# Optimization experiments

Hardware: AMD Instinct MI355X
Metric: run time of the kernel (lower is better)

Reference implementation:

```python
import jax, jax.numpy as jnp
from jax import lax
import numpy as np

B, H, W, C = 16, 128, 256, 64
D = 12            # local_max_disp // stride
H_OUT, W_OUT = 1024, 2048


def setup_inputs() -> dict:
    key = jax.random.key(0)
    ks = jax.random.split(key, 8)
    feat_l = jax.random.normal(ks[0], (B, H, W, C), dtype=jnp.float32)
    feat_r = jax.random.normal(ks[1], (B, H, W, C), dtype=jnp.float32)
    def conv_w(k, shape):
        fan_in = shape[0] * shape[1] * shape[2] * shape[3]
        return jax.random.normal(k, shape, dtype=jnp.float32) / np.sqrt(fan_in)
    return {
        'feat_l': feat_l, 'feat_r': feat_r,
        'w0': conv_w(ks[2], (3, 3, 3, 1, 4)), 'b0': jnp.zeros((4,), jnp.float32),
        'w1': conv_w(ks[3], (3, 3, 3, 4, 4)), 'b1': jnp.zeros((4,), jnp.float32),
        'w2': conv_w(ks[4], (3, 3, 3, 4, 4)), 'b2': jnp.zeros((4,), jnp.float32),
        'w3': conv_w(ks[5], (3, 3, 3, 4, 4)), 'b3': jnp.zeros((4,), jnp.float32),
        'wf': conv_w(ks[6], (3, 3, 3, 4, 1)), 'bf': jnp.zeros((1,), jnp.float32),
    }


def _cost_volume(feat_l, feat_r, max_disp, stride):
    # For disparity i: cost[:, :, w, i] = sum_c |L[b,h,w,c] - R[b,h,w-i,c]| for w >= i,
    # and sum_c |L[b,h,w,c]| for w < i (which equals diff against a zero-padded shift of R).
    planes = []
    for i in range(0, max_disp, stride):
        if i == 0:
            r_shift = feat_r
        else:
            r_shift = jnp.pad(feat_r[:, :, :-i, :], ((0, 0), (0, 0), (i, 0), (0, 0)))
        planes.append(jnp.sum(jnp.abs(feat_l - r_shift), axis=-1))
    return jnp.stack(planes, axis=-1)  # [B,H,W,D]


def _conv3d(x, w, b):
    # x: [B,H,W,D,C_in], w: [3,3,3,C_in,C_out]
    y = lax.conv_general_dilated(x, w, (1, 1, 1), 'SAME',
                                 dimension_numbers=('NHWDC', 'HWDIO', 'NHWDC'))
    return y + b


def reference(feat_l, feat_r, w0, b0, w1, b1, w2, b2, w3, b3, wf, bf):
    cost = _cost_volume(feat_l, feat_r, D, 1)          # [B,H,W,D]
    x = cost[..., None]                                 # [B,H,W,D,1]
    x = jax.nn.relu(_conv3d(x, w0, b0))
    x = jax.nn.relu(_conv3d(x, w1, b1))
    x = jax.nn.relu(_conv3d(x, w2, b2))
    x = jax.nn.relu(_conv3d(x, w3, b3))
    x = _conv3d(x, wf, bf)                              # [B,H,W,D,1]
    cost = x[..., 0]                                    # [B,H,W,D]
    sm = jax.nn.softmax(-cost, axis=-1)
    disp = jnp.arange(D, dtype=jnp.float32)
    pred = jnp.sum(sm * disp, axis=-1, keepdims=True)   # [B,H,W,1]
    out = jax.image.resize(pred, (pred.shape[0], H_OUT, W_OUT, 1), method='bilinear')
    return out
```

## Files before the change

### kernel.cpp

```cpp
#include <hip/hip_runtime.h>
#include <cstddef>

#define BB   16
#define HHY  128
#define WWX  256
#define CC   64
#define DDp  12
#define HOUT 1024
#define WOUT 2048

typedef _Float16 hf;
typedef __fp16 h2 __attribute__((ext_vector_type(2)));

__device__ __forceinline__ h2 u2h(unsigned u) { return __builtin_bit_cast(h2, u); }
__device__ __forceinline__ unsigned pkrtz(float a, float b) {
  return __builtin_bit_cast(unsigned, __builtin_amdgcn_cvt_pkrtz(a, b));
}

#if defined(__has_builtin)
#if __has_builtin(__builtin_amdgcn_fdot2)
#define FDOT2(a, b, c) __builtin_amdgcn_fdot2((a), (b), (c), false)
#endif
#endif
#ifndef FDOT2
#define FDOT2(a, b, c) ((float)(a)[0] * (float)(b)[0] + (float)(a)[1] * (float)(b)[1] + (c))
#endif

__device__ __forceinline__ float adot(unsigned lu, unsigned ru, float c) {
  const h2 d = u2h(lu) - u2h(ru);
  const unsigned au = __builtin_bit_cast(unsigned, d) & 0x7FFF7FFFu;
  return FDOT2(u2h(au), u2h(0x3C003C00u), c);
}

__global__ __launch_bounds__(256) void prep_k(const float* __restrict__ w1,
                                              const float* __restrict__ w2,
                                              const float* __restrict__ w3,
                                              const float* __restrict__ wf,
                                              hf* __restrict__ o) {
  const int t = threadIdx.x;
  for (int i = t; i < 432; i += 256) {
    const int t27 = i >> 4;
    const int ci = (i >> 2) & 3;
    const int co = i & 3;
    const int dst = (t27 * 4 + co) * 4 + ci;
    o[dst]       = (hf)w1[i];
    o[432 + dst] = (hf)w2[i];
    o[864 + dst] = (hf)w3[i];
  }
  for (int i = t; i < 108; i += 256) o[1296 + i] = (hf)wf[i];
}

#define RSTRIDE 36

__global__ __launch_bounds__(256) void cost_volume_k(const float* __restrict__ L,
                                                     const float* __restrict__ R,
                                                     float* __restrict__ cost) {
  __shared__ unsigned lsR[WWX * RSTRIDE];
  const int t = threadIdx.x;
  const int h = blockIdx.x;
  const int b = blockIdx.y;
  const size_t rowbase = ((size_t)(b * HHY + h)) * WWX;
  const float* Lrow = L + rowbase * CC;
  const float* Rrow = R + rowbase * CC;

#pragma unroll
  for (int j = 0; j < 16; ++j) {
    const int fi = t + 256 * j;
    const int w = fi >> 4;
    const int f4 = fi & 15;
    const float4 v = *(const float4*)(Rrow + (size_t)w * CC + 4 * f4);
    *(uint2*)(&lsR[w * RSTRIDE + f4 * 2]) =
        make_uint2(pkrtz(v.x, v.y), pkrtz(v.z, v.w));
  }

  unsigned lh[32];
#pragma unroll
  for (int k = 0; k < 16; ++k) {
    const float4 v = *(const float4*)(Lrow + (size_t)t * CC + 4 * k);
    lh[2 * k]     = pkrtz(v.x, v.y);
    lh[2 * k + 1] = pkrtz(v.z, v.w);
  }

  float sl = 0.f;
#pragma unroll
  for (int i = 0; i < 32; ++i) sl = adot(lh[i], 0u, sl);

  __syncthreads();

  float acc[DDp];
#pragma unroll
  for (int d = 0; d < DDp; ++d) {
    if (t >= d) {
      const unsigned* rp = &lsR[(t - d) * RSTRIDE];
      float a = 0.f;
#pragma unroll
      for (int k = 0; k < 8; ++k) {
        const uint4 r = *(const uint4*)(rp + 4 * k);
        a = adot(lh[4 * k + 0], r.x, a);
        a = adot(lh[4 * k + 1], r.y, a);
        a = adot(lh[4 * k + 2], r.z, a);
        a = adot(lh[4 * k + 3], r.w, a);
      }
      acc[d] = a;
    } else {
      acc[d] = sl;
    }
  }

  float* cp = cost + (rowbase + t) * DDp;
#pragma unroll
  for (int d = 0; d < DDp; d += 4)
    *(float4*)(cp + d) = make_float4(acc[d], acc[d + 1], acc[d + 2], acc[d + 3]);
}

__global__ __launch_bounds__(256) void conv0_k(const float* __restrict__ x,
                                               const float* __restrict__ wt,
                                               const float* __restrict__ bs,
                                               hf* __restrict__ y) {
  constexpr int S = 20;
  __shared__ float ls[WWX * S];
  const int t = threadIdx.x;
  const int id = blockIdx.x;
  const int h = ((id & 7) << 4) | ((id >> 3) & 15);
  const int b = id >> 7;

  float acc[DDp][4];
#pragma unroll
  for (int co = 0; co < 4; ++co) {
    const float bv = bs[co];
#pragma unroll
    for (int d = 0; d < DDp; ++d) acc[d][co] = bv;
  }

#pragma unroll
  for (int kh = 0; kh < 3; ++kh) {
    const int hh = h + kh - 1;
    if (hh < 0 || hh >= HHY) continue;

    __syncthreads();
    const float* xr = x + ((size_t)(b * HHY + hh) * WWX) * DDp;
#pragma unroll
    for (int j = 0; j < 3; ++j) {
      const int fi4 = t + 256 * j;
      const int w_ = fi4 / 3;
      const int k_ = fi4 - w_ * 3;
      *(float4*)(&ls[w_ * S + k_ * 4]) = ((const float4*)xr)[fi4];
    }
    __syncthreads();

#pragma unroll
    for (int kw = 0; kw < 3; ++kw) {
      const int ww = t + kw - 1;
      if (ww < 0 || ww >= WWX) continue;
      const float* lp = &ls[ww * S];

      const float* wp = wt + (size_t)(kh * 3 + kw) * 12;
      float wr[12];
#pragma unroll
      for (int i = 0; i < 12; ++i) wr[i] = wp[i];

      float v[DDp];
#pragma unroll
      for (int k = 0; k < 3; ++k)
        ((float4*)v)[k] = *(const float4*)(lp + 4 * k);
#pragma unroll
      for (int vo = 0; vo < DDp; ++vo)
#pragma unroll
        for (int kd = 0; kd < 3; ++kd) {
          const int d = vo + 1 - kd;
          if (d < 0 || d >= DDp) continue;
#pragma unroll
          for (int co = 0; co < 4; ++co)
            acc[d][co] += v[vo] * wr[kd * 4 + co];
        }
    }
  }

  unsigned ov[DDp * 2];
#pragma unroll
  for (int d = 0; d < DDp; ++d) {
    ov[d * 2]     = pkrtz(fmaxf(acc[d][0], 0.f), fmaxf(acc[d][1], 0.f));
    ov[d * 2 + 1] = pkrtz(fmaxf(acc[d][2], 0.f), fmaxf(acc[d][3], 0.f));
  }
  uint4* yp = (uint4*)(y + ((size_t)(b * HHY + h) * WWX + t) * (DDp * 4));
#pragma unroll
  for (int i = 0; i < 6; ++i) yp[i] = ((uint4*)ov)[i];
}

template <int COUT, bool FUSE_SM>
__global__ __launch_bounds__(256) void convh_k(const hf* __restrict__ x,
                                               const hf* __restrict__ wh,
                                               const float* __restrict__ bs,
                                               void* __restrict__ yv) {
  constexpr int DCH = DDp * 4;
  constexpr int SU  = 26;
  __shared__ unsigned lsu[WWX * SU];

  const int t = threadIdx.x;
  const int id = blockIdx.x;
  const int h = ((id & 7) << 4) | ((id >> 3) & 15);
  const int b = id >> 7;

  float acc[DDp][COUT];
#pragma unroll
  for (int co = 0; co < COUT; ++co) {
    const float bv = bs[co];
#pragma unroll
    for (int d = 0; d < DDp; ++d) acc[d][co] = bv;
  }

  const unsigned* whu = (const unsigned*)wh;

#pragma unroll
  for (int kh = 0; kh < 3; ++kh) {
    const int hh = h + kh - 1;
    if (hh < 0 || hh >= HHY) continue;

    __syncthreads();
    const uint4* xr = (const uint4*)(x + (size_t)(b * HHY + hh) * WWX * DCH);
#pragma unroll
    for (int j = 0; j < 6; ++j) {
      const int fi4 = t + 256 * j;
      const int w_ = fi4 / 6;
      const int k_ = fi4 - w_ * 6;
      const uint4 v = xr[fi4];
      unsigned* dst = &lsu[w_ * SU + k_ * 4];
      *(uint2*)(dst)     = make_uint2(v.x, v.y);
      *(uint2*)(dst + 2) = make_uint2(v.z, v.w);
    }
    __syncthreads();

#pragma unroll
    for (int kw = 0; kw < 3; ++kw) {
      const int ww = t + kw - 1;
      if (ww < 0 || ww >= WWX) continue;

      unsigned w01[3][COUT], w23[3][COUT];
      const int tap3 = (kh * 3 + kw) * 3;
#pragma unroll
      for (int kd = 0; kd < 3; ++kd)
#pragma unroll
        for (int co = 0; co < COUT; ++co) {
          const int u0 = ((tap3 + kd) * COUT + co) * 2;
          w01[kd][co] = whu[u0];
          w23[kd][co] = whu[u0 + 1];
        }

      const unsigned* lp = &lsu[ww * SU];
#pragma unroll
      for (int vo = 0; vo < DDp; ++vo) {
        const uint2 xu = *(const uint2*)(lp + vo * 2);
        const h2 x01 = u2h(xu.x), x23 = u2h(xu.y);
#pragma unroll
        for (int kd = 0; kd < 3; ++kd) {
          const int d = vo + 1 - kd;
          if (d < 0 || d >= DDp) continue;
#pragma unroll
          for (int co = 0; co < COUT; ++co)
            acc[d][co] = FDOT2(x01, u2h(w01[kd][co]),
                         FDOT2(x23, u2h(w23[kd][co]), acc[d][co]));
        }
      }
    }
  }

  if constexpr (FUSE_SM) {
    float* y = (float*)yv;
    float mn = acc[0][0];
#pragma unroll
    for (int d = 1; d < DDp; ++d) mn = fminf(mn, acc[d][0]);
    float s = 0.f, sw = 0.f;
#pragma unroll
    for (int d = 0; d < DDp; ++d) {
      const float e = __expf(mn - acc[d][0]);
      s += e;
      sw += e * (float)d;
    }
    y[(size_t)(b * HHY + h) * WWX + t] = sw / s;
  } else {
    hf* y = (hf*)yv;
    unsigned ov[DDp * 2];
#pragma unroll
    for (int d = 0; d < DDp; ++d) {
      ov[d * 2]     = pkrtz(fmaxf(acc[d][0], 0.f), fmaxf(acc[d][1 % COUT], 0.f));
      ov[d * 2 + 1] = pkrtz(fmaxf(acc[d][2 % COUT], 0.f), fmaxf(acc[d][3 % COUT], 0.f));
    }
    uint4* yp = (uint4*)(y + ((size_t)(b * HHY + h) * WWX + t) * DCH);
#pragma unroll
    for (int i = 0; i < 6; ++i) yp[i] = ((uint4*)ov)[i];
  }
}

__global__ __launch_bounds__(256) void resize4_k(const float* __restrict__ pred,
                                                 float* __restrict__ out) {
  const int idx = blockIdx.x * 256 + threadIdx.x;
  const int xg = idx & 511;
  const int y = (idx >> 9) & 1023;
  const int b = idx >> 19;

  const int parity = xg & 1;
  const int m = xg >> 1;
  const int x0 = m - 1 + parity;
  const int x0c = max(x0, 0);
  const int x1c = min(x0 + 1, WWX - 1);
  const float wx0 = (parity ? 0.0625f : 0.5625f);

  const int py = y & 7;
  const int my = y >> 3;
  const int y0 = my - 1 + (py >= 4 ? 1 : 0);
  const float wy = (py >= 4) ? 0.0625f + (py - 4) * 0.125f : 0.5625f + py * 0.125f;
  const int y0c = max(y0, 0);
  const int y1c = min(y0 + 1, HHY - 1);

  const float* pb = pred + (size_t)b * HHY * WWX;
  const float a = pb[y0c * WWX + x0c];
  const float bv = pb[y0c * WWX + x1c];
  const float c = pb[y1c * WWX + x0c];
  const float d = pb[y1c * WWX + x1c];

  const float top0 = a + (bv - a) * wx0;
  const float bot0 = c + (d - c) * wx0;
  const float dtop = (bv - a) * 0.125f;
  const float dbot = (d - c) * 0.125f;

  float4 o;
  o.x = top0 + wy * (bot0 - top0);
  o.y = (top0 + dtop) + wy * ((bot0 + dbot) - (top0 + dtop));
  o.z = (top0 + 2.f * dtop) + wy * ((bot0 + 2.f * dbot) - (top0 + 2.f * dtop));
  o.w = (top0 + 3.f * dtop) + wy * ((bot0 + 3.f * dbot) - (top0 + 3.f * dtop));

  *(float4*)(out + (size_t)idx * 4) = o;
}

extern "C" void kernel_launch(void* const* d_in, const int* in_sizes, int n_in,
                              void* d_out, int out_size, void* d_ws, size_t ws_size,
                              hipStream_t stream) {
  const float* feat_l = (const float*)d_in[0];
  const float* feat_r = (const float*)d_in[1];
  const float* w0 = (const float*)d_in[2];
  const float* b0 = (const float*)d_in[3];
  const float* w1 = (const float*)d_in[4];
  const float* b1 = (const float*)d_in[5];
  const float* w2 = (const float*)d_in[6];
  const float* b2 = (const float*)d_in[7];
  const float* w3 = (const float*)d_in[8];
  const float* b3 = (const float*)d_in[9];
  const float* wf = (const float*)d_in[10];
  const float* bf = (const float*)d_in[11];
  float* out = (float*)d_out;

  char* ws = (char*)d_ws;
  hf*    A  = (hf*)ws;
  hf*    Bf = (hf*)(ws + 50331648);
  float* C  = (float*)(ws + 100663296);
  float* P  = (float*)(ws + 125829120);
  hf*    Wh = (hf*)(ws + 127926272);

  dim3 blk(256);
  prep_k<<<dim3(1), blk, 0, stream>>>(w1, w2, w3, wf, Wh);
  cost_volume_k<<<dim3(HHY, BB), blk, 0, stream>>>(feat_l, feat_r, C);
  conv0_k<<<dim3(HHY * BB), blk, 0, stream>>>(C, w0, b0, A);
  convh_k<4, false><<<dim3(HHY * BB), blk, 0, stream>>>(A,  Wh,        b1, Bf);
  convh_k<4, false><<<dim3(HHY * BB), blk, 0, stream>>>(Bf, Wh + 432,  b2, A);
  convh_k<4, false><<<dim3(HHY * BB), blk, 0, stream>>>(A,  Wh + 864,  b3, Bf);
  convh_k<1, true ><<<dim3(HHY * BB), blk, 0, stream>>>(Bf, Wh + 1296, bf, P);

  const int ngroups = BB * HOUT * (WOUT / 4);
  resize4_k<<<dim3(ngroups / 256), blk, 0, stream>>>(P, out);
}
```

Baseline: 299.5 us.

## Tile cost volume along width and split disparities across thread groups

The cost volume kernel now launches one block per 64-column tile of a row instead of one per full row, staging the R halo and the L tile as fp16 in shared memory. Each thread computes three disparities for one column rather than twelve, and results are transposed through LDS for coalesced float4 stores. The goal is more blocks, less LDS per block and fewer registers, which raises occupancy and shortens per-thread serial work. In exchange, L rows are re-read from LDS by four thread groups, the R halo is loaded redundantly per tile, and two extra barriers are added.

```diff
diff --git a/kernel.cpp b/kernel.cpp
--- a/kernel.cpp
+++ b/kernel.cpp
@@ -50,67 +50,75 @@
   for (int i = t; i < 108; i += 256) o[1296 + i] = (hf)wf[i];
 }
 
-#define RSTRIDE 36
-
-__global__ __launch_bounds__(256) void cost_volume_k(const float* __restrict__ L,
-                                                     const float* __restrict__ R,
-                                                     float* __restrict__ cost) {
-  __shared__ unsigned lsR[WWX * RSTRIDE];
+#define CVS 36
+#define CVHALO 11
+#define CVWT 64
+#define CVROWS (CVWT + CVHALO + CVWT)
+
+__global__ __launch_bounds__(256, 8) void cost_volume_k(const float* __restrict__ L,
+                                                        const float* __restrict__ R,
+                                                        float* __restrict__ cost) {
+  __shared__ unsigned ls[CVROWS * CVS];
   const int t = threadIdx.x;
-  const int h = blockIdx.x;
-  const int b = blockIdx.y;
+  const int wb = blockIdx.x * CVWT;
+  const int h = blockIdx.y;
+  const int b = blockIdx.z;
   const size_t rowbase = ((size_t)(b * HHY + h)) * WWX;
   const float* Lrow = L + rowbase * CC;
   const float* Rrow = R + rowbase * CC;
 
 #pragma unroll
-  for (int j = 0; j < 16; ++j) {
+  for (int j = 0; j < 9; ++j) {
     const int fi = t + 256 * j;
-    const int w = fi >> 4;
-    const int f4 = fi & 15;
-    const float4 v = *(const float4*)(Rrow + (size_t)w * CC + 4 * f4);
-    *(uint2*)(&lsR[w * RSTRIDE + f4 * 2]) =
-        make_uint2(pkrtz(v.x, v.y), pkrtz(v.z, v.w));
-  }
-
-  unsigned lh[32];
-#pragma unroll
-  for (int k = 0; k < 16; ++k) {
-    const float4 v = *(const float4*)(Lrow + (size_t)t * CC + 4 * k);
-    lh[2 * k]     = pkrtz(v.x, v.y);
-    lh[2 * k + 1] = pkrtz(v.z, v.w);
-  }
-
-  float sl = 0.f;
-#pragma unroll
-  for (int i = 0; i < 32; ++i) sl = adot(lh[i], 0u, sl);
-
+    if (fi < CVROWS * 16) {
+      const int row = fi >> 4;
+      const int f4 = fi & 15;
+      float4 v = make_float4(0.f, 0.f, 0.f, 0.f);
+      if (row < CVWT + CVHALO) {
+        const int gw = wb - CVHALO + row;
+        if (gw >= 0) v = *(const float4*)(Rrow + (size_t)gw * CC + 4 * f4);
+      } else {
+        const int gw = wb + row - (CVWT + CVHALO);
+        v = *(const float4*)(Lrow + (size_t)gw * CC + 4 * f4);
+      }
+      *(uint2*)(&ls[row * CVS + f4 * 2]) =
+          make_uint2(pkrtz(v.x, v.y), pkrtz(v.z, v.w));
+    }
+  }
   __syncthreads();
 
-  float acc[DDp];
-#pragma unroll
-  for (int d = 0; d < DDp; ++d) {
-    if (t >= d) {
-      const unsigned* rp = &lsR[(t - d) * RSTRIDE];
-      float a = 0.f;
-#pragma unroll
-      for (int k = 0; k < 8; ++k) {
-        const uint4 r = *(const uint4*)(rp + 4 * k);
-        a = adot(lh[4 * k + 0], r.x, a);
-        a = adot(lh[4 * k + 1], r.y, a);
-        a = adot(lh[4 * k + 2], r.z, a);
-        a = adot(lh[4 * k + 3], r.w, a);
-      }
-      acc[d] = a;
-    } else {
-      acc[d] = sl;
-    }
-  }
-
-  float* cp = cost + (rowbase + t) * DDp;
-#pragma unroll
-  for (int d = 0; d < DDp; d += 4)
-    *(float4*)(cp + d) = make_float4(acc[d], acc[d + 1], acc[d + 2], acc[d + 3]);
+  const int w = t & 63;
+  const int dg = t >> 6;
+  const int rb0 = (w + CVHALO - dg) * CVS;
+  const int rb1 = (w + CVHALO - dg - 4) * CVS;
+  const int rb2 = (w + CVHALO - dg - 8) * CVS;
+  const int rbL = (CVWT + CVHALO + w) * CVS;
+
+  float a0 = 0.f, a1 = 0.f, a2 = 0.f;
+#pragma unroll
+  for (int k = 0; k < 8; ++k) {
+    const uint4 lq = *(const uint4*)(&ls[rbL + 4 * k]);
+    const uint4 r0 = *(const uint4*)(&ls[rb0 + 4 * k]);
+    a0 = adot(lq.x, r0.x, a0); a0 = adot(lq.y, r0.y, a0);
+    a0 = adot(lq.z, r0.z, a0); a0 = adot(lq.w, r0.w, a0);
+    const uint4 r1 = *(const uint4*)(&ls[rb1 + 4 * k]);
+    a1 = adot(lq.x, r1.x, a1); a1 = adot(lq.y, r1.y, a1);
+    a1 = adot(lq.z, r1.z, a1); a1 = adot(lq.w, r1.w, a1);
+    const uint4 r2 = *(const uint4*)(&ls[rb2 + 4 * k]);
+    a2 = adot(lq.x, r2.x, a2); a2 = adot(lq.y, r2.y, a2);
+    a2 = adot(lq.z, r2.z, a2); a2 = adot(lq.w, r2.w, a2);
+  }
+
+  __syncthreads();
+  float* lo = (float*)ls;
+  lo[w * DDp + dg]     = a0;
+  lo[w * DDp + dg + 4] = a1;
+  lo[w * DDp + dg + 8] = a2;
+  __syncthreads();
+  if (t < CVWT * DDp / 4) {
+    const float4 v = *(const float4*)(&lo[4 * t]);
+    *(float4*)(cost + (rowbase + wb) * DDp + 4 * t) = v;
+  }
 }
 
 __global__ __launch_bounds__(256) void conv0_k(const float* __restrict__ x,
@@ -358,7 +366,7 @@
 
   dim3 blk(256);
   prep_k<<<dim3(1), blk, 0, stream>>>(w1, w2, w3, wf, Wh);
-  cost_volume_k<<<dim3(HHY, BB), blk, 0, stream>>>(feat_l, feat_r, C);
+  cost_volume_k<<<dim3(WWX / CVWT, HHY, BB), blk, 0, stream>>>(feat_l, feat_r, C);
   conv0_k<<<dim3(HHY * BB), blk, 0, stream>>>(C, w0, b0, A);
   convh_k<4, false><<<dim3(HHY * BB), blk, 0, stream>>>(A,  Wh,        b1, Bf);
   convh_k<4, false><<<dim3(HHY * BB), blk, 0, stream>>>(Bf, Wh + 432,  b2, A);
```

Result: no change. 295.8 us (-1.2%).

## Double-buffer cost-volume tiles through LDS with async global-to-LDS loads

Applied to the files above, without the earlier changes.

The cost-volume kernel is restructured so that each block walks through 16 tiles of 64 columns. The next tile's left and right features, with an 11-column halo of the right image, are prefetched into a second LDS buffer using global_load_lds while the current tile is computed. LDS rows use an XOR swizzle to avoid bank conflicts, and the arithmetic moves from packed fp16 dot products to plain fp32 absolute differences. Output is staged through LDS so global stores are coalesced float4 writes. The costs are re-reading the halo columns, a larger LDS footprint per block, fewer blocks overall, and more barriers per tile.

```diff
diff --git a/kernel.cpp b/kernel.cpp
--- a/kernel.cpp
+++ b/kernel.cpp
@@ -50,67 +50,111 @@
   for (int i = t; i < 108; i += 256) o[1296 + i] = (hf)wf[i];
 }
 
-#define RSTRIDE 36
+#define CVS2 64
+#define CVHALO 11
+#define CVWT 64
+#define CVREAL (CVWT + CVHALO + CVWT)
+#define CVROWP 140
+#define CVT2 16
+
+#define CV_ISSUE(TAU, BSEL) do {                                              \
+    const int wt_ = (TAU) & 3;                                                \
+    const int hh_ = ((TAU) >> 2) & (HHY - 1);                                 \
+    const int bb_ = (TAU) >> 9;                                               \
+    const size_t rb_ = ((size_t)(bb_ * HHY + hh_)) * WWX;                     \
+    const float* Lr_ = L + rb_ * CC;                                          \
+    const float* Rr_ = R + rb_ * CC;                                          \
+    const int wb_ = wt_ * CVWT;                                               \
+    _Pragma("unroll")                                                         \
+    for (int i_ = 0; i_ < 9; ++i_) {                                          \
+      const int G_ = wv * 9 + i_;                                             \
+      if (G_ < 35) {                                                          \
+        const int g_ = G_ * 64 + w;                                           \
+        const int row_ = g_ >> 4;                                             \
+        const int sl_ = g_ & 15;                                              \
+        const int sc_ = sl_ ^ (row_ & 15);                                    \
+        const float* src_;                                                    \
+        if (row_ < CVWT + CVHALO) {                                           \
+          int gw_ = wb_ - CVHALO + row_; if (gw_ < 0) gw_ = 0;                \
+          src_ = Rr_ + (size_t)gw_ * CC + sc_ * 4;                            \
+        } else {                                                              \
+          int lr_ = row_ - (CVWT + CVHALO); if (lr_ > 63) lr_ = 63;           \
+          src_ = Lr_ + (size_t)(wb_ + lr_) * CC + sc_ * 4;                    \
+        }                                                                     \
+        __builtin_amdgcn_global_load_lds(                                     \
+            src_, &buf[(BSEL) * (CVROWP * CVS2) + G_ * 256], 16, 0, 0);       \
+      }                                                                       \
+    }                                                                         \
+  } while (0)
 
 __global__ __launch_bounds__(256) void cost_volume_k(const float* __restrict__ L,
                                                      const float* __restrict__ R,
                                                      float* __restrict__ cost) {
-  __shared__ unsigned lsR[WWX * RSTRIDE];
+  __shared__ __align__(16) float buf[2 * CVROWP * CVS2];
+  __shared__ float lot[2 * CVWT * 13];
   const int t = threadIdx.x;
-  const int h = blockIdx.x;
-  const int b = blockIdx.y;
-  const size_t rowbase = ((size_t)(b * HHY + h)) * WWX;
-  const float* Lrow = L + rowbase * CC;
-  const float* Rrow = R + rowbase * CC;
-
-#pragma unroll
-  for (int j = 0; j < 16; ++j) {
-    const int fi = t + 256 * j;
-    const int w = fi >> 4;
-    const int f4 = fi & 15;
-    const float4 v = *(const float4*)(Rrow + (size_t)w * CC + 4 * f4);
-    *(uint2*)(&lsR[w * RSTRIDE + f4 * 2]) =
-        make_uint2(pkrtz(v.x, v.y), pkrtz(v.z, v.w));
-  }
-
-  unsigned lh[32];
-#pragma unroll
-  for (int k = 0; k < 16; ++k) {
-    const float4 v = *(const float4*)(Lrow + (size_t)t * CC + 4 * k);
-    lh[2 * k]     = pkrtz(v.x, v.y);
-    lh[2 * k + 1] = pkrtz(v.z, v.w);
-  }
-
-  float sl = 0.f;
-#pragma unroll
-  for (int i = 0; i < 32; ++i) sl = adot(lh[i], 0u, sl);
-
-  __syncthreads();
-
-  float acc[DDp];
-#pragma unroll
-  for (int d = 0; d < DDp; ++d) {
-    if (t >= d) {
-      const unsigned* rp = &lsR[(t - d) * RSTRIDE];
-      float a = 0.f;
-#pragma unroll
-      for (int k = 0; k < 8; ++k) {
-        const uint4 r = *(const uint4*)(rp + 4 * k);
-        a = adot(lh[4 * k + 0], r.x, a);
-        a = adot(lh[4 * k + 1], r.y, a);
-        a = adot(lh[4 * k + 2], r.z, a);
-        a = adot(lh[4 * k + 3], r.w, a);
-      }
-      acc[d] = a;
+  const int w = t & 63;
+  const int dg = t >> 6;
+  const int wv = dg;
+  const int base = blockIdx.x * CVT2;
+
+  CV_ISSUE(base, 0);
+
+  for (int k = 0; k < CVT2; ++k) {
+    const int tau = base + k;
+
+    if (k + 1 < CVT2) {
+      CV_ISSUE(tau + 1, (k + 1) & 1);
+      asm volatile("s_waitcnt vmcnt(8)" ::: "memory");
     } else {
-      acc[d] = sl;
-    }
-  }
-
-  float* cp = cost + (rowbase + t) * DDp;
-#pragma unroll
-  for (int d = 0; d < DDp; d += 4)
-    *(float4*)(cp + d) = make_float4(acc[d], acc[d + 1], acc[d + 2], acc[d + 3]);
+      asm volatile("s_waitcnt vmcnt(0)" ::: "memory");
+    }
+    __builtin_amdgcn_s_barrier();
+
+    const float* bp = &buf[(k & 1) * (CVROWP * CVS2)];
+    const int r0 = w + CVHALO - dg;
+    const int r1 = r0 - 4;
+    const int r2 = r0 - 8;
+    const int rL = CVWT + CVHALO + w;
+
+    float a0 = 0.f, a1 = 0.f, a2 = 0.f, sl = 0.f;
+#pragma unroll
+    for (int kk = 0; kk < 16; ++kk) {
+      const float4 lq = *(const float4*)&bp[rL * 64 + ((kk ^ (rL & 15)) << 2)];
+      const float4 q0 = *(const float4*)&bp[r0 * 64 + ((kk ^ (r0 & 15)) << 2)];
+      a0 += fabsf(lq.x - q0.x) + fabsf(lq.y - q0.y) +
+            fabsf(lq.z - q0.z) + fabsf(lq.w - q0.w);
+      const float4 q1 = *(const float4*)&bp[r1 * 64 + ((kk ^ (r1 & 15)) << 2)];
+      a1 += fabsf(lq.x - q1.x) + fabsf(lq.y - q1.y) +
+            fabsf(lq.z - q1.z) + fabsf(lq.w - q1.w);
+      const float4 q2 = *(const float4*)&bp[r2 * 64 + ((kk ^ (r2 & 15)) << 2)];
+      a2 += fabsf(lq.x - q2.x) + fabsf(lq.y - q2.y) +
+            fabsf(lq.z - q2.z) + fabsf(lq.w - q2.w);
+      sl += fabsf(lq.x) + fabsf(lq.y) + fabsf(lq.z) + fabsf(lq.w);
+    }
+
+    const int wt = tau & 3;
+    const int hh = (tau >> 2) & (HHY - 1);
+    const int bb = tau >> 9;
+    const int wg = wt * CVWT + w;
+    if (wg < dg)     a0 = sl;
+    if (wg < dg + 4) a1 = sl;
+    if (wg < dg + 8) a2 = sl;
+
+    float* lo = &lot[(k & 1) * CVWT * 13];
+    lo[w * 13 + dg]     = a0;
+    lo[w * 13 + dg + 4] = a1;
+    lo[w * 13 + dg + 8] = a2;
+    asm volatile("s_waitcnt lgkmcnt(0)" ::: "memory");
+    __builtin_amdgcn_s_barrier();
+    if (t < CVWT * DDp / 4) {
+      const int wq = t / 3;
+      const int q  = t - wq * 3;
+      const float4 v = *(const float4*)(&lo[wq * 13 + 4 * q]);
+      const size_t rowbase = ((size_t)(bb * HHY + hh)) * WWX;
+      *(float4*)(cost + (rowbase + wt * CVWT) * DDp + 4 * t) = v;
+    }
+  }
 }
 
 __global__ __launch_bounds__(256) void conv0_k(const float* __restrict__ x,
@@ -358,7 +402,7 @@
 
   dim3 blk(256);
   prep_k<<<dim3(1), blk, 0, stream>>>(w1, w2, w3, wf, Wh);
-  cost_volume_k<<<dim3(HHY, BB), blk, 0, stream>>>(feat_l, feat_r, C);
+  cost_volume_k<<<dim3(BB * HHY * (WWX / CVWT) / CVT2), blk, 0, stream>>>(feat_l, feat_r, C);
   conv0_k<<<dim3(HHY * BB), blk, 0, stream>>>(C, w0, b0, A);
   convh_k<4, false><<<dim3(HHY * BB), blk, 0, stream>>>(A,  Wh,        b1, Bf);
   convh_k<4, false><<<dim3(HHY * BB), blk, 0, stream>>>(Bf, Wh + 432,  b2, A);
```

New measurement: 299.8 us. Within noise of the previous version (+0.1%).
